# Kernel optimization log

Measured on AMD Instinct MI355X. Metric: run time of the kernel, lower is better.

The kernel has to match this reference:

```python
import jax, jax.numpy as jnp
import numpy as np

IN_CH = 4
HIDDEN = 32
NNODES = 4
N_NODES_TOTAL = 4_000_000
N_EDGES = 12_000_000


def setup_inputs() -> dict:
    key = jax.random.key(0)
    ks = jax.random.split(key, 8)
    state = jax.random.normal(ks[0], (N_NODES_TOTAL, IN_CH), dtype=jnp.float32)
    edge_index = jax.random.randint(ks[1], (2, N_EDGES), 0, N_NODES_TOTAL, dtype=jnp.int64)
    s = 1.0 / np.sqrt(IN_CH)
    W_gcn = jax.random.uniform(ks[2], (IN_CH, HIDDEN), jnp.float32, -s, s)
    b_gcn = jnp.zeros((HIDDEN,), jnp.float32)
    d_in1 = IN_CH + HIDDEN
    s1 = 1.0 / np.sqrt(d_in1)
    W1 = jax.random.uniform(ks[3], (d_in1, HIDDEN), jnp.float32, -s1, s1)
    b1 = jax.random.uniform(ks[4], (HIDDEN,), jnp.float32, -s1, s1)
    s2 = 1.0 / np.sqrt(HIDDEN)
    W2 = jax.random.uniform(ks[5], (HIDDEN, 1), jnp.float32, -s2, s2)
    b2 = jax.random.uniform(ks[6], (1,), jnp.float32, -s2, s2)
    return {"state": state, "edge_index": edge_index, "W_gcn": W_gcn,
            "b_gcn": b_gcn, "W1": W1, "b1": b1, "W2": W2, "b2": b2}


def gcn_conv(x, edge_index, W, b):
    # PyG GCNConv: linear transform, add self-loops, symmetric deg normalization,
    # scatter-add messages src -> dst, then bias.
    N = x.shape[0]
    loops = jnp.arange(N, dtype=edge_index.dtype)
    src = jnp.concatenate([edge_index[0], loops])
    dst = jnp.concatenate([edge_index[1], loops])
    xw = x @ W  # [N, HIDDEN]
    deg = jnp.zeros((N,), xw.dtype).at[dst].add(jnp.ones((), xw.dtype))
    dinv = jax.lax.rsqrt(deg)  # deg >= 1 thanks to self-loops
    norm = dinv[src] * dinv[dst]  # [E+N]
    out = jnp.zeros_like(xw).at[dst].add(norm[:, None] * xw[src])
    return out + b


def reference(state, edge_index, W_gcn, b_gcn, W1, b1, W2, b2):
    x_pp = gcn_conv(state, edge_index, W_gcn, b_gcn)          # [N, HIDDEN]
    x_pp = jnp.concatenate([state, x_pp], axis=1)              # [N, IN_CH+HIDDEN]
    x_pp = x_pp.reshape(-1, NNODES, IN_CH + HIDDEN)            # [B, nnodes, F]
    v = jnp.sum(x_pp, axis=1)                                  # [B, F] sum-pool over nodes
    v = jax.nn.relu(v @ W1 + b1)
    v = v @ W2 + b2
    return v.squeeze(-1)                                       # [B]
```

## Files before the change

kernel.cpp:

```cpp
#include <hip/hip_runtime.h>
#include <hip/hip_cooperative_groups.h>

namespace cg = cooperative_groups;

typedef unsigned long long u64;
typedef __attribute__((ext_vector_type(4))) int i32x4;
typedef __attribute__((ext_vector_type(2))) unsigned long long u64x2;

#define N_NODES   4000000
#define N_EDGES   12000000
#define N_GRAPHS  1000000

#define NBIN      977
#define GPBIN     1024
#define NPBIN     4096
#define BINCAP    14336
#define LCAP      16
#define SBLOCKS   256
#define SEPB      46880


__global__ __launch_bounds__(256) void fold_kernel(
    const float* __restrict__ Wgcn, const float* __restrict__ bgcn,
    const float* __restrict__ W1, const float* __restrict__ b1,
    float* __restrict__ fold) {
  int t = threadIdx.x;
  if (t < 128) {
    int j = t >> 2, c = t & 3;
    float s = 0.f;
    for (int k = 0; k < 32; ++k) s += Wgcn[c * 32 + k] * W1[(4 + k) * 32 + j];
    fold[j * 4 + c] = s;
  }
  if (t < 32) {
    float s = 0.f;
    for (int k = 0; k < 32; ++k) s += bgcn[k] * W1[(4 + k) * 32 + t];
    fold[128 + t] = b1[t] + 4.0f * s;
  }
}


__global__ __launch_bounds__(512) void binscatter_kernel(
    const int* __restrict__ src, const int* __restrict__ dst,
    unsigned* __restrict__ gcur, u64* __restrict__ recs) {
  extern __shared__ char smem[];
  u64* buf = (u64*)smem;
  unsigned* cnt = (unsigned*)(smem + NBIN * LCAP * 8);
  int t = threadIdx.x;
  for (int i = t; i < NBIN; i += 512) cnt[i] = 0;
  __syncthreads();
  const int base = blockIdx.x * SEPB;
  const int limit = min(SEPB, N_EDGES - base);
  const int V = limit >> 2;
  const i32x4* src4 = (const i32x4*)(src + base);
  const i32x4* dst4 = (const i32x4*)(dst + base);
  const int nrounds = (V + 1023) / 1024;

  i32x4 cs0 = {0,0,0,0}, cd0 = {0,0,0,0}, cs1 = {0,0,0,0}, cd1 = {0,0,0,0};
  {
    int i0 = t, i1 = t + 512;
    if (i0 < V) { cs0 = __builtin_nontemporal_load(src4 + i0);
                  cd0 = __builtin_nontemporal_load(dst4 + i0); }
    if (i1 < V) { cs1 = __builtin_nontemporal_load(src4 + i1);
                  cd1 = __builtin_nontemporal_load(dst4 + i1); }
  }
  for (int r = 0; r < nrounds; ++r) {
    i32x4 ns0 = {0,0,0,0}, nd0 = {0,0,0,0}, ns1 = {0,0,0,0}, nd1 = {0,0,0,0};
    if (r + 1 < nrounds) {
      int j0 = (r + 1) * 1024 + t, j1 = j0 + 512;
      if (j0 < V) { ns0 = __builtin_nontemporal_load(src4 + j0);
                    nd0 = __builtin_nontemporal_load(dst4 + j0); }
      if (j1 < V) { ns1 = __builtin_nontemporal_load(src4 + j1);
                    nd1 = __builtin_nontemporal_load(dst4 + j1); }
    }
    int idx0 = r * 1024 + t;
#pragma unroll
    for (int half = 0; half < 2; ++half) {
      int idx = idx0 + half * 512;
      if (idx < V) {
        i32x4 vs = half ? cs1 : cs0;
        i32x4 vd = half ? cd1 : cd0;
#pragma unroll
        for (int k = 0; k < 4; ++k) {
          int s = vs[k];
          int d = vd[k];
          unsigned graph = (unsigned)d >> 2;
          unsigned bin   = graph >> 10;
          unsigned glo   = graph & 1023u;
          u64 rec = ((u64)glo << 32) | ((u64)((unsigned)s << 2) | (unsigned)(d & 3));
          unsigned pos = atomicAdd(&cnt[bin], 1u);
          if (pos < LCAP) buf[bin * LCAP + pos] = rec;
          else {
            unsigned p = atomicAdd(&gcur[bin], 1u);
            if (p < BINCAP) recs[(size_t)bin * BINCAP + p] = rec;
          }
        }
      }
    }
    __syncthreads();
    bool fin = (r == nrounds - 1);
    for (int bin = t; bin < NBIN; bin += 512) {
      unsigned c = cnt[bin]; if (c > LCAP) c = LCAP;
      unsigned nn = fin ? c : (c & ~7u);
      if (nn) {
        unsigned pos = atomicAdd(&gcur[bin], nn);
        if (pos + nn <= BINCAP) {
          u64* dp = recs + (size_t)bin * BINCAP + pos;
          for (unsigned i2 = 0; i2 < nn; ++i2) dp[i2] = buf[bin * LCAP + i2];
        }
      }
      unsigned rem2 = c - nn;
      for (unsigned i2 = 0; i2 < rem2; ++i2)
        buf[bin * LCAP + i2] = buf[bin * LCAP + nn + i2];
      cnt[bin] = rem2;
    }
    __syncthreads();
    cs0 = ns0; cd0 = nd0; cs1 = ns1; cd1 = nd1;
  }
}


__global__ __launch_bounds__(512, 8) void fusedreduce_kernel(
    const u64* __restrict__ recs, const unsigned* __restrict__ gcur,
    float4* __restrict__ dsi4, const float4* __restrict__ state4,
    const float* __restrict__ W1, const float* __restrict__ fold,
    const float* __restrict__ W2, const float* __restrict__ b2,
    float* __restrict__ out) {
  extern __shared__ float dynsm[];
  unsigned* degL = (unsigned*)dynsm;
  float* dinvL = dynsm;
  float* accL  = dynsm + NPBIN;
  __shared__ float4 w1aT[32], wg1T[32];
  __shared__ float b1p[32], w2s[32];
  int t = threadIdx.x, bin = blockIdx.x;
  if (t < 32) {
    w1aT[t] = make_float4(W1[t], W1[32 + t], W1[64 + t], W1[96 + t]);
    wg1T[t] = ((const float4*)fold)[t];
    b1p[t]  = fold[128 + t];
    w2s[t]  = W2[t];
  }
  for (int i = t; i < NPBIN; i += 512) { degL[i] = 0u; accL[i] = 0.f; }
  __syncthreads();
  unsigned n = gcur[bin]; if (n > BINCAP) n = BINCAP;
  const u64* rp = recs + (size_t)bin * BINCAP;
  {
    const u64x2* rv = (const u64x2*)rp;
    unsigned nv = n >> 1;
    for (unsigned i = t; i < nv; i += 512) {
      u64x2 p = __builtin_nontemporal_load(rv + i);
      atomicAdd(&degL[((unsigned)(p.x >> 32)) * 4 + ((unsigned)p.x & 3u)], 1u);
      atomicAdd(&degL[((unsigned)(p.y >> 32)) * 4 + ((unsigned)p.y & 3u)], 1u);
    }
    if ((n & 1u) && t == 0) {
      u64 v = rp[n - 1];
      atomicAdd(&degL[((unsigned)(v >> 32)) * 4 + ((unsigned)v & 3u)], 1u);
    }
  }
  __syncthreads();
  int nb = bin * NPBIN;
  for (int i = t; i < NPBIN; i += 512) {
    int node = nb + i;
    float dv = rsqrtf((float)(degL[i] + 1u));
    dinvL[i] = dv;
    if (node < N_NODES) {
      float4 s = state4[node];
      dsi4[node] = make_float4(dv * s.x, dv * s.y, dv * s.z, dv * s.w);
    }
  }
  __threadfence();
  cg::this_grid().sync();
  unsigned q = n >> 2;
  for (unsigned i = t; i < q; i += 512) {
    u64 r0 = __builtin_nontemporal_load(rp + i);
    u64 r1 = __builtin_nontemporal_load(rp + i + q);
    u64 r2 = __builtin_nontemporal_load(rp + i + 2 * q);
    u64 r3 = __builtin_nontemporal_load(rp + i + 3 * q);
    unsigned lo0 = (unsigned)r0, g0 = (unsigned)(r0 >> 32), s0 = lo0 >> 2;
    unsigned lo1 = (unsigned)r1, g1 = (unsigned)(r1 >> 32), s1 = lo1 >> 2;
    unsigned lo2 = (unsigned)r2, g2 = (unsigned)(r2 >> 32), s2 = lo2 >> 2;
    unsigned lo3 = (unsigned)r3, g3 = (unsigned)(r3 >> 32), s3 = lo3 >> 2;
    float w0 = dinvL[g0 * 4 + (lo0 & 3u)];
    float w1 = dinvL[g1 * 4 + (lo1 & 3u)];
    float w2 = dinvL[g2 * 4 + (lo2 & 3u)];
    float w3 = dinvL[g3 * 4 + (lo3 & 3u)];
    float4 m0 = dsi4[s0], m1 = dsi4[s1], m2 = dsi4[s2], m3 = dsi4[s3];
    float* a;
    a = accL + g0 * 4;
    atomicAdd(a + 0, w0 * m0.x); atomicAdd(a + 1, w0 * m0.y);
    atomicAdd(a + 2, w0 * m0.z); atomicAdd(a + 3, w0 * m0.w);
    a = accL + g1 * 4;
    atomicAdd(a + 0, w1 * m1.x); atomicAdd(a + 1, w1 * m1.y);
    atomicAdd(a + 2, w1 * m1.z); atomicAdd(a + 3, w1 * m1.w);
    a = accL + g2 * 4;
    atomicAdd(a + 0, w2 * m2.x); atomicAdd(a + 1, w2 * m2.y);
    atomicAdd(a + 2, w2 * m2.z); atomicAdd(a + 3, w2 * m2.w);
    a = accL + g3 * 4;
    atomicAdd(a + 0, w3 * m3.x); atomicAdd(a + 1, w3 * m3.y);
    atomicAdd(a + 2, w3 * m3.z); atomicAdd(a + 3, w3 * m3.w);
  }
  {
    unsigned done = q << 2;
    unsigned rem = n - done;
    if ((unsigned)t < rem) {
      u64 v = rp[done + t];
      unsigned lo = (unsigned)v, g = (unsigned)(v >> 32), s = lo >> 2;
      float w = dinvL[g * 4 + (lo & 3u)];
      float4 mm = dsi4[s];
      float* a = accL + g * 4;
      atomicAdd(a + 0, w * mm.x); atomicAdd(a + 1, w * mm.y);
      atomicAdd(a + 2, w * mm.z); atomicAdd(a + 3, w * mm.w);
    }
  }
  __syncthreads();
  for (int gi = t; gi < GPBIN; gi += 512) {
    int g = bin * GPBIN + gi;
    if (g >= N_GRAPHS) break;
    float4 s0 = state4[4 * g + 0], s1 = state4[4 * g + 1];
    float4 s2 = state4[4 * g + 2], s3 = state4[4 * g + 3];
    float d0 = dinvL[gi * 4 + 0], d1 = dinvL[gi * 4 + 1];
    float d2 = dinvL[gi * 4 + 2], d3 = dinvL[gi * 4 + 3];
    float q0 = d0 * d0, q1 = d1 * d1, q2 = d2 * d2, q3 = d3 * d3;
    float ax = accL[gi * 4 + 0] + q0 * s0.x + q1 * s1.x + q2 * s2.x + q3 * s3.x;
    float ay = accL[gi * 4 + 1] + q0 * s0.y + q1 * s1.y + q2 * s2.y + q3 * s3.y;
    float az = accL[gi * 4 + 2] + q0 * s0.z + q1 * s1.z + q2 * s2.z + q3 * s3.z;
    float aw = accL[gi * 4 + 3] + q0 * s0.w + q1 * s1.w + q2 * s2.w + q3 * s3.w;
    float vx = s0.x + s1.x + s2.x + s3.x;
    float vy = s0.y + s1.y + s2.y + s3.y;
    float vz = s0.z + s1.z + s2.z + s3.z;
    float vw = s0.w + s1.w + s2.w + s3.w;
    float accum = b2[0];
#pragma unroll 4
    for (int j = 0; j < 32; ++j) {
      float4 wa = w1aT[j], wg = wg1T[j];
      float h = b1p[j]
              + vx * wa.x + vy * wa.y + vz * wa.z + vw * wa.w
              + ax * wg.x + ay * wg.y + az * wg.z + aw * wg.w;
      accum += fmaxf(h, 0.f) * w2s[j];
    }
    out[g] = accum;
  }
}


__global__ __launch_bounds__(512) void bindeg_kernel(
    const u64* __restrict__ recs, const unsigned* __restrict__ gcur,
    const float4* __restrict__ state4,
    float* __restrict__ dinv, float4* __restrict__ dsi4) {
  __shared__ unsigned degL[NPBIN];
  int t = threadIdx.x, bin = blockIdx.x;
  for (int i = t; i < NPBIN; i += 512) degL[i] = 0;
  __syncthreads();
  unsigned n = gcur[bin]; if (n > BINCAP) n = BINCAP;
  const u64* rp = recs + (size_t)bin * BINCAP;
  const u64x2* rv = (const u64x2*)rp;
  unsigned nv = n >> 1;
  for (unsigned i = t; i < nv; i += 512) {
    u64x2 p = __builtin_nontemporal_load(rv + i);
    atomicAdd(&degL[((unsigned)(p.x >> 32)) * 4 + ((unsigned)p.x & 3u)], 1u);
    atomicAdd(&degL[((unsigned)(p.y >> 32)) * 4 + ((unsigned)p.y & 3u)], 1u);
  }
  if ((n & 1u) && t == 0) {
    u64 v = rp[n - 1];
    atomicAdd(&degL[((unsigned)(v >> 32)) * 4 + ((unsigned)v & 3u)], 1u);
  }
  __syncthreads();
  int nb = bin * NPBIN;
  for (int i = t; i < NPBIN; i += 512) {
    int node = nb + i;
    if (node < N_NODES) {
      float dv = rsqrtf((float)(degL[i] + 1u));
      dinv[node] = dv;
      float4 s = state4[node];
      dsi4[node] = make_float4(dv * s.x, dv * s.y, dv * s.z, dv * s.w);
    }
  }
}

__global__ __launch_bounds__(512, 8) void binreduce_kernel(
    const u64* __restrict__ recs, const unsigned* __restrict__ gcur,
    const float* __restrict__ dinv, const float4* __restrict__ dsi4,
    const float4* __restrict__ state4,
    const float* __restrict__ W1, const float* __restrict__ fold,
    const float* __restrict__ W2, const float* __restrict__ b2,
    float* __restrict__ out) {
  extern __shared__ float dynsm[];
  float* dinvL = dynsm;
  float* accL  = dynsm + NPBIN;
  __shared__ float4 w1aT[32], wg1T[32];
  __shared__ float b1p[32], w2s[32];
  int t = threadIdx.x, bin = blockIdx.x;
  if (t < 32) {
    w1aT[t] = make_float4(W1[t], W1[32 + t], W1[64 + t], W1[96 + t]);
    wg1T[t] = ((const float4*)fold)[t];
    b1p[t]  = fold[128 + t];
    w2s[t]  = W2[t];
  }
  int nb = bin * NPBIN;
  for (int i = t; i < NPBIN; i += 512) {
    int node = nb + i;
    dinvL[i] = (node < N_NODES) ? dinv[node] : 0.f;
    accL[i]  = 0.f;
  }
  __syncthreads();
  unsigned n = gcur[bin]; if (n > BINCAP) n = BINCAP;
  const u64* rp = recs + (size_t)bin * BINCAP;
  unsigned q = n >> 2;
  for (unsigned i = t; i < q; i += 512) {
    u64 r0 = __builtin_nontemporal_load(rp + i);
    u64 r1 = __builtin_nontemporal_load(rp + i + q);
    u64 r2 = __builtin_nontemporal_load(rp + i + 2 * q);
    u64 r3 = __builtin_nontemporal_load(rp + i + 3 * q);
    unsigned lo0 = (unsigned)r0, g0 = (unsigned)(r0 >> 32), s0 = lo0 >> 2;
    unsigned lo1 = (unsigned)r1, g1 = (unsigned)(r1 >> 32), s1 = lo1 >> 2;
    unsigned lo2 = (unsigned)r2, g2 = (unsigned)(r2 >> 32), s2 = lo2 >> 2;
    unsigned lo3 = (unsigned)r3, g3 = (unsigned)(r3 >> 32), s3 = lo3 >> 2;
    float w0 = dinvL[g0 * 4 + (lo0 & 3u)];
    float w1 = dinvL[g1 * 4 + (lo1 & 3u)];
    float w2 = dinvL[g2 * 4 + (lo2 & 3u)];
    float w3 = dinvL[g3 * 4 + (lo3 & 3u)];
    float4 m0 = dsi4[s0], m1 = dsi4[s1], m2 = dsi4[s2], m3 = dsi4[s3];
    float* a;
    a = accL + g0 * 4;
    atomicAdd(a + 0, w0 * m0.x); atomicAdd(a + 1, w0 * m0.y);
    atomicAdd(a + 2, w0 * m0.z); atomicAdd(a + 3, w0 * m0.w);
    a = accL + g1 * 4;
    atomicAdd(a + 0, w1 * m1.x); atomicAdd(a + 1, w1 * m1.y);
    atomicAdd(a + 2, w1 * m1.z); atomicAdd(a + 3, w1 * m1.w);
    a = accL + g2 * 4;
    atomicAdd(a + 0, w2 * m2.x); atomicAdd(a + 1, w2 * m2.y);
    atomicAdd(a + 2, w2 * m2.z); atomicAdd(a + 3, w2 * m2.w);
    a = accL + g3 * 4;
    atomicAdd(a + 0, w3 * m3.x); atomicAdd(a + 1, w3 * m3.y);
    atomicAdd(a + 2, w3 * m3.z); atomicAdd(a + 3, w3 * m3.w);
  }
  unsigned done = q << 2;
  unsigned rem = n - done;
  if ((unsigned)t < rem) {
    u64 v = rp[done + t];
    unsigned lo = (unsigned)v, g = (unsigned)(v >> 32), s = lo >> 2;
    float w = dinvL[g * 4 + (lo & 3u)];
    float4 mm = dsi4[s];
    float* a = accL + g * 4;
    atomicAdd(a + 0, w * mm.x); atomicAdd(a + 1, w * mm.y);
    atomicAdd(a + 2, w * mm.z); atomicAdd(a + 3, w * mm.w);
  }
  __syncthreads();
  for (int gi = t; gi < GPBIN; gi += 512) {
    int g = bin * GPBIN + gi;
    if (g >= N_GRAPHS) break;
    float4 s0 = state4[4 * g + 0], s1 = state4[4 * g + 1];
    float4 s2 = state4[4 * g + 2], s3 = state4[4 * g + 3];
    float d0 = dinvL[gi * 4 + 0], d1 = dinvL[gi * 4 + 1];
    float d2 = dinvL[gi * 4 + 2], d3 = dinvL[gi * 4 + 3];
    float q0 = d0 * d0, q1 = d1 * d1, q2 = d2 * d2, q3 = d3 * d3;
    float ax = accL[gi * 4 + 0] + q0 * s0.x + q1 * s1.x + q2 * s2.x + q3 * s3.x;
    float ay = accL[gi * 4 + 1] + q0 * s0.y + q1 * s1.y + q2 * s2.y + q3 * s3.y;
    float az = accL[gi * 4 + 2] + q0 * s0.z + q1 * s1.z + q2 * s2.z + q3 * s3.z;
    float aw = accL[gi * 4 + 3] + q0 * s0.w + q1 * s1.w + q2 * s2.w + q3 * s3.w;
    float vx = s0.x + s1.x + s2.x + s3.x;
    float vy = s0.y + s1.y + s2.y + s3.y;
    float vz = s0.z + s1.z + s2.z + s3.z;
    float vw = s0.w + s1.w + s2.w + s3.w;
    float accum = b2[0];
#pragma unroll 4
    for (int j = 0; j < 32; ++j) {
      float4 wa = w1aT[j], wg = wg1T[j];
      float h = b1p[j]
              + vx * wa.x + vy * wa.y + vz * wa.z + vw * wa.w
              + ax * wg.x + ay * wg.y + az * wg.z + aw * wg.w;
      accum += fmaxf(h, 0.f) * w2s[j];
    }
    out[g] = accum;
  }
}


__global__ __launch_bounds__(256) void deg_kernel(
    const i32x4* __restrict__ dst4, unsigned* __restrict__ deg) {
  int stride = gridDim.x * blockDim.x;
  for (int e = blockIdx.x * blockDim.x + threadIdx.x; e < N_EDGES / 4; e += stride) {
    i32x4 d = __builtin_nontemporal_load(dst4 + e);
    atomicAdd(&deg[d.x], 1u); atomicAdd(&deg[d.y], 1u);
    atomicAdd(&deg[d.z], 1u); atomicAdd(&deg[d.w], 1u);
  }
}

__global__ __launch_bounds__(256) void dinv_kernel(unsigned* __restrict__ degdinv) {
  int i = blockIdx.x * blockDim.x + threadIdx.x;
  if (i < N_NODES) {
    float dv = rsqrtf((float)(degdinv[i] + 1u));
    reinterpret_cast<float*>(degdinv)[i] = dv;
  }
}

__global__ __launch_bounds__(256) void scatter_kernel(
    const i32x4* __restrict__ src4, const i32x4* __restrict__ dst4,
    const float* __restrict__ dinv, const float4* __restrict__ state4,
    float* __restrict__ acc) {
  int stride = gridDim.x * blockDim.x;
  for (int e = blockIdx.x * blockDim.x + threadIdx.x; e < N_EDGES / 4; e += stride) {
    i32x4 s4 = __builtin_nontemporal_load(src4 + e);
    i32x4 d4 = __builtin_nontemporal_load(dst4 + e);
#pragma unroll
    for (int u = 0; u < 4; ++u) {
      int s = (u == 0) ? s4.x : (u == 1) ? s4.y : (u == 2) ? s4.z : s4.w;
      int d = (u == 0) ? d4.x : (u == 1) ? d4.y : (u == 2) ? d4.z : d4.w;
      float w = dinv[s] * dinv[d];
      float4 st = state4[s];
      float* base = acc + (size_t)(d >> 2) * 4;
      atomicAdd(base + 0, w * st.x); atomicAdd(base + 1, w * st.y);
      atomicAdd(base + 2, w * st.z); atomicAdd(base + 3, w * st.w);
    }
  }
}

__global__ __launch_bounds__(256) void final_kernel(
    const float4* __restrict__ state4, const float4* __restrict__ dinv4,
    const float4* __restrict__ acc4, const float* __restrict__ W1,
    const float* __restrict__ fold, const float* __restrict__ W2,
    const float* __restrict__ b2, float* __restrict__ out) {
  __shared__ float4 w1aT[32], wg1T[32];
  __shared__ float b1p[32], w2s[32];
  int t = threadIdx.x;
  if (t < 32) {
    w1aT[t] = make_float4(W1[t], W1[32 + t], W1[64 + t], W1[96 + t]);
    wg1T[t] = ((const float4*)fold)[t];
    b1p[t]  = fold[128 + t];
    w2s[t]  = W2[t];
  }
  __syncthreads();
  int b = blockIdx.x * blockDim.x + t;
  if (b >= N_GRAPHS) return;
  float4 s0 = state4[4 * b + 0], s1 = state4[4 * b + 1];
  float4 s2 = state4[4 * b + 2], s3 = state4[4 * b + 3];
  float4 dv = dinv4[b];
  float4 a  = acc4[b];
  float q0 = dv.x * dv.x, q1 = dv.y * dv.y, q2 = dv.z * dv.z, q3 = dv.w * dv.w;
  a.x += q0 * s0.x + q1 * s1.x + q2 * s2.x + q3 * s3.x;
  a.y += q0 * s0.y + q1 * s1.y + q2 * s2.y + q3 * s3.y;
  a.z += q0 * s0.z + q1 * s1.z + q2 * s2.z + q3 * s3.z;
  a.w += q0 * s0.w + q1 * s1.w + q2 * s2.w + q3 * s3.w;
  float4 vs;
  vs.x = s0.x + s1.x + s2.x + s3.x;
  vs.y = s0.y + s1.y + s2.y + s3.y;
  vs.z = s0.z + s1.z + s2.z + s3.z;
  vs.w = s0.w + s1.w + s2.w + s3.w;
  float accum = b2[0];
#pragma unroll
  for (int j = 0; j < 32; ++j) {
    float4 wa = w1aT[j], wg = wg1T[j];
    float h = b1p[j]
            + vs.x * wa.x + vs.y * wa.y + vs.z * wa.z + vs.w * wa.w
            + a.x * wg.x + a.y * wg.y + a.z * wg.z + a.w * wg.w;
    accum += fmaxf(h, 0.f) * w2s[j];
  }
  out[b] = accum;
}


extern "C" void kernel_launch(void* const* d_in, const int* in_sizes, int n_in,
                              void* d_out, int out_size, void* d_ws, size_t ws_size,
                              hipStream_t stream) {
  const float* state = (const float*)d_in[0];
  const int*   ei    = (const int*)d_in[1];
  const float* Wgcn  = (const float*)d_in[2];
  const float* bgcn  = (const float*)d_in[3];
  const float* W1    = (const float*)d_in[4];
  const float* b1    = (const float*)d_in[5];
  const float* W2    = (const float*)d_in[6];
  const float* b2    = (const float*)d_in[7];
  float* out = (float*)d_out;

  char* ws = (char*)d_ws;
  const size_t MB = 1024u * 1024u;

  const size_t recs_bytes = (size_t)NBIN * BINCAP * 8;
  const size_t dinv_off   = recs_bytes;
  const size_t dsi_off    = dinv_off + (size_t)N_NODES * 4;
  const size_t gcur_off   = (dsi_off + (size_t)N_NODES * 16 + 255) & ~(size_t)255;
  const size_t need_bin   = gcur_off + 8192 + 1024;

  const size_t scat_smem = (size_t)NBIN * LCAP * 8 + NBIN * 4;
  const size_t red_smem  = 2 * NPBIN * 4;

  if (ws_size >= need_bin) {
    const u64*      recs = (const u64*)ws;
    u64*            recsw = (u64*)ws;
    float*          dinv = (float*)(ws + dinv_off);
    float4*         dsi4 = (float4*)(ws + dsi_off);
    unsigned*       gcur = (unsigned*)(ws + gcur_off);
    float*          fold = (float*)(ws + gcur_off + 8192);
    const float4*   state4 = (const float4*)state;

    (void)hipMemsetAsync(gcur, 0, 8192, stream);
    fold_kernel<<<1, 128, 0, stream>>>(Wgcn, bgcn, W1, b1, fold);
    binscatter_kernel<<<SBLOCKS, 512, scat_smem, stream>>>(
        ei, ei + N_EDGES, gcur, recsw);

    bool coop_ok = false;
    {
      int dev = 0;
      (void)hipGetDevice(&dev);
      int coop_attr = 0;
      (void)hipDeviceGetAttribute(&coop_attr, hipDeviceAttributeCooperativeLaunch, dev);
      int numCU = 0;
      (void)hipDeviceGetAttribute(&numCU, hipDeviceAttributeMultiprocessorCount, dev);
      int maxblk = 0;
      hipError_t oe = hipOccupancyMaxActiveBlocksPerMultiprocessor(
          &maxblk, fusedreduce_kernel, 512, red_smem);
      if (coop_attr && oe == hipSuccess && (long)maxblk * numCU >= NBIN) {
        const float* W1p = W1; const float* foldp = fold;
        const float* W2p = W2; const float* b2p = b2;
        void* args[] = {(void*)&recs, (void*)&gcur, (void*)&dsi4, (void*)&state4,
                        (void*)&W1p, (void*)&foldp, (void*)&W2p, (void*)&b2p,
                        (void*)&out};
        hipError_t le = hipLaunchCooperativeKernel(
            fusedreduce_kernel, dim3(NBIN), dim3(512), args,
            (unsigned)red_smem, stream);
        coop_ok = (le == hipSuccess);
      }
    }
    if (!coop_ok) {
      bindeg_kernel<<<NBIN, 512, 0, stream>>>(recs, gcur, state4, dinv, dsi4);
      binreduce_kernel<<<NBIN, 512, red_smem, stream>>>(
          recs, gcur, dinv, dsi4, state4, W1, fold, W2, b2, out);
    }
    return;
  }

  {
    unsigned* deg  = (unsigned*)ws;
    float*    acc  = (float*)(ws + 16 * MB);
    float*    fold = (float*)(ws + 32 * MB);
    (void)hipMemsetAsync(d_ws, 0, 32 * MB + 1024, stream);
    fold_kernel<<<1, 128, 0, stream>>>(Wgcn, bgcn, W1, b1, fold);
    deg_kernel<<<4096, 256, 0, stream>>>((const i32x4*)(ei + N_EDGES), deg);
    dinv_kernel<<<(N_NODES + 255) / 256, 256, 0, stream>>>(deg);
    scatter_kernel<<<8192, 256, 0, stream>>>(
        (const i32x4*)ei, (const i32x4*)(ei + N_EDGES),
        (const float*)deg, (const float4*)state, acc);
    final_kernel<<<(N_GRAPHS + 255) / 256, 256, 0, stream>>>(
        (const float4*)state, (const float4*)deg, (const float4*)acc,
        W1, fold, W2, b2, out);
  }
}
```

Before: 429.7 us.

## Pack edge records into 32-bit words with finer 256-graph sub-bins

Edge records shrink from 64-bit to 32-bit words by packing the local graph id (8 bits), source node and slot into one word. Bins are subdivided into 3907 sub-bins of 256 graphs each, which the reduce kernels read four at a time as quads. This halves the record traffic written by the scatter and read twice by the reduce. The cost is many more shared-memory staging bins with a smaller per-bin buffer (LCAP 9) and a larger shared allocation, which may mean more small global flushes and lower scatter occupancy.

```diff
diff --git a/kernel.cpp b/kernel.cpp
--- a/kernel.cpp
+++ b/kernel.cpp
@@ -3,21 +3,19 @@
 
 namespace cg = cooperative_groups;
 
-typedef unsigned long long u64;
 typedef __attribute__((ext_vector_type(4))) int i32x4;
-typedef __attribute__((ext_vector_type(2))) unsigned long long u64x2;
 
 #define N_NODES   4000000
 #define N_EDGES   12000000
 #define N_GRAPHS  1000000
 
-#define NBIN      977
-#define GPBIN     1024
-#define NPBIN     4096
-#define BINCAP    14336
-#define LCAP      16
+#define NMB       3907
+#define MBCAP     4096
+#define LCAP      9
 #define SBLOCKS   256
 #define SEPB      46880
+#define NQUAD     977
+
 
 
 __global__ __launch_bounds__(256) void fold_kernel(
@@ -41,12 +39,12 @@
 
 __global__ __launch_bounds__(512) void binscatter_kernel(
     const int* __restrict__ src, const int* __restrict__ dst,
-    unsigned* __restrict__ gcur, u64* __restrict__ recs) {
+    unsigned* __restrict__ gcur, unsigned* __restrict__ recs) {
   extern __shared__ char smem[];
-  u64* buf = (u64*)smem;
-  unsigned* cnt = (unsigned*)(smem + NBIN * LCAP * 8);
+  unsigned* buf = (unsigned*)smem;
+  unsigned* cnt = (unsigned*)(smem + NMB * LCAP * 4);
   int t = threadIdx.x;
-  for (int i = t; i < NBIN; i += 512) cnt[i] = 0;
+  for (int i = t; i < NMB; i += 512) cnt[i] = 0;
   __syncthreads();
   const int base = blockIdx.x * SEPB;
   const int limit = min(SEPB, N_EDGES - base);
@@ -81,30 +79,29 @@
         i32x4 vd = half ? cd1 : cd0;
 #pragma unroll
         for (int k = 0; k < 4; ++k) {
-          int s = vs[k];
-          int d = vd[k];
-          unsigned graph = (unsigned)d >> 2;
-          unsigned bin   = graph >> 10;
-          unsigned glo   = graph & 1023u;
-          u64 rec = ((u64)glo << 32) | ((u64)((unsigned)s << 2) | (unsigned)(d & 3));
+          unsigned s = (unsigned)vs[k];
+          unsigned d = (unsigned)vd[k];
+          unsigned graph = d >> 2;
+          unsigned bin   = graph >> 8;
+          unsigned rec = ((graph & 255u) << 24) | (s << 2) | (d & 3u);
           unsigned pos = atomicAdd(&cnt[bin], 1u);
           if (pos < LCAP) buf[bin * LCAP + pos] = rec;
           else {
             unsigned p = atomicAdd(&gcur[bin], 1u);
-            if (p < BINCAP) recs[(size_t)bin * BINCAP + p] = rec;
+            if (p < MBCAP) recs[(size_t)bin * MBCAP + p] = rec;
           }
         }
       }
     }
     __syncthreads();
     bool fin = (r == nrounds - 1);
-    for (int bin = t; bin < NBIN; bin += 512) {
+    for (int bin = t; bin < NMB; bin += 512) {
       unsigned c = cnt[bin]; if (c > LCAP) c = LCAP;
       unsigned nn = fin ? c : (c & ~7u);
       if (nn) {
         unsigned pos = atomicAdd(&gcur[bin], nn);
-        if (pos + nn <= BINCAP) {
-          u64* dp = recs + (size_t)bin * BINCAP + pos;
+        if (pos + nn <= MBCAP) {
+          unsigned* dp = recs + (size_t)bin * MBCAP + pos;
           for (unsigned i2 = 0; i2 < nn; ++i2) dp[i2] = buf[bin * LCAP + i2];
         }
       }
@@ -120,7 +117,7 @@
 
 
 __global__ __launch_bounds__(512, 8) void fusedreduce_kernel(
-    const u64* __restrict__ recs, const unsigned* __restrict__ gcur,
+    const unsigned* __restrict__ recs, const unsigned* __restrict__ gcur,
     float4* __restrict__ dsi4, const float4* __restrict__ state4,
     const float* __restrict__ W1, const float* __restrict__ fold,
     const float* __restrict__ W2, const float* __restrict__ b2,
@@ -128,36 +125,41 @@
   extern __shared__ float dynsm[];
   unsigned* degL = (unsigned*)dynsm;
   float* dinvL = dynsm;
-  float* accL  = dynsm + NPBIN;
+  float* accL  = dynsm + 4096;
   __shared__ float4 w1aT[32], wg1T[32];
   __shared__ float b1p[32], w2s[32];
-  int t = threadIdx.x, bin = blockIdx.x;
+  int t = threadIdx.x, qb = blockIdx.x;
   if (t < 32) {
     w1aT[t] = make_float4(W1[t], W1[32 + t], W1[64 + t], W1[96 + t]);
     wg1T[t] = ((const float4*)fold)[t];
     b1p[t]  = fold[128 + t];
     w2s[t]  = W2[t];
   }
-  for (int i = t; i < NPBIN; i += 512) { degL[i] = 0u; accL[i] = 0.f; }
-  __syncthreads();
-  unsigned n = gcur[bin]; if (n > BINCAP) n = BINCAP;
-  const u64* rp = recs + (size_t)bin * BINCAP;
-  {
-    const u64x2* rv = (const u64x2*)rp;
-    unsigned nv = n >> 1;
-    for (unsigned i = t; i < nv; i += 512) {
-      u64x2 p = __builtin_nontemporal_load(rv + i);
-      atomicAdd(&degL[((unsigned)(p.x >> 32)) * 4 + ((unsigned)p.x & 3u)], 1u);
-      atomicAdd(&degL[((unsigned)(p.y >> 32)) * 4 + ((unsigned)p.y & 3u)], 1u);
-    }
-    if ((n & 1u) && t == 0) {
-      u64 v = rp[n - 1];
-      atomicAdd(&degL[((unsigned)(v >> 32)) * 4 + ((unsigned)v & 3u)], 1u);
-    }
-  }
-  __syncthreads();
-  int nb = bin * NPBIN;
-  for (int i = t; i < NPBIN; i += 512) {
+  for (int i = t; i < 4096; i += 512) { degL[i] = 0u; accL[i] = 0.f; }
+  __syncthreads();
+  unsigned n[4];
+  const unsigned* rp[4];
+#pragma unroll
+  for (int s = 0; s < 4; ++s) {
+    int mb = qb * 4 + s;
+    unsigned c = (mb < NMB) ? gcur[mb] : 0u;
+    n[s] = (c > MBCAP) ? (unsigned)MBCAP : c;
+    rp[s] = recs + (size_t)mb * MBCAP;
+  }
+  unsigned mx = max(max(n[0], n[1]), max(n[2], n[3]));
+  for (unsigned i = t; i < mx; i += 512) {
+#pragma unroll
+    for (int s = 0; s < 4; ++s) {
+      if (i < n[s]) {
+        unsigned r = __builtin_nontemporal_load(rp[s] + i);
+        unsigned lg = (unsigned)(s * 256) + (r >> 24);
+        atomicAdd(&degL[lg * 4 + (r & 3u)], 1u);
+      }
+    }
+  }
+  __syncthreads();
+  int nb = qb * 4096;
+  for (int i = t; i < 4096; i += 512) {
     int node = nb + i;
     float dv = rsqrtf((float)(degL[i] + 1u));
     dinvL[i] = dv;
@@ -168,51 +170,49 @@
   }
   __threadfence();
   cg::this_grid().sync();
-  unsigned q = n >> 2;
-  for (unsigned i = t; i < q; i += 512) {
-    u64 r0 = __builtin_nontemporal_load(rp + i);
-    u64 r1 = __builtin_nontemporal_load(rp + i + q);
-    u64 r2 = __builtin_nontemporal_load(rp + i + 2 * q);
-    u64 r3 = __builtin_nontemporal_load(rp + i + 3 * q);
-    unsigned lo0 = (unsigned)r0, g0 = (unsigned)(r0 >> 32), s0 = lo0 >> 2;
-    unsigned lo1 = (unsigned)r1, g1 = (unsigned)(r1 >> 32), s1 = lo1 >> 2;
-    unsigned lo2 = (unsigned)r2, g2 = (unsigned)(r2 >> 32), s2 = lo2 >> 2;
-    unsigned lo3 = (unsigned)r3, g3 = (unsigned)(r3 >> 32), s3 = lo3 >> 2;
-    float w0 = dinvL[g0 * 4 + (lo0 & 3u)];
-    float w1 = dinvL[g1 * 4 + (lo1 & 3u)];
-    float w2 = dinvL[g2 * 4 + (lo2 & 3u)];
-    float w3 = dinvL[g3 * 4 + (lo3 & 3u)];
-    float4 m0 = dsi4[s0], m1 = dsi4[s1], m2 = dsi4[s2], m3 = dsi4[s3];
-    float* a;
-    a = accL + g0 * 4;
-    atomicAdd(a + 0, w0 * m0.x); atomicAdd(a + 1, w0 * m0.y);
-    atomicAdd(a + 2, w0 * m0.z); atomicAdd(a + 3, w0 * m0.w);
-    a = accL + g1 * 4;
-    atomicAdd(a + 0, w1 * m1.x); atomicAdd(a + 1, w1 * m1.y);
-    atomicAdd(a + 2, w1 * m1.z); atomicAdd(a + 3, w1 * m1.w);
-    a = accL + g2 * 4;
-    atomicAdd(a + 0, w2 * m2.x); atomicAdd(a + 1, w2 * m2.y);
-    atomicAdd(a + 2, w2 * m2.z); atomicAdd(a + 3, w2 * m2.w);
-    a = accL + g3 * 4;
-    atomicAdd(a + 0, w3 * m3.x); atomicAdd(a + 1, w3 * m3.y);
-    atomicAdd(a + 2, w3 * m3.z); atomicAdd(a + 3, w3 * m3.w);
-  }
-  {
-    unsigned done = q << 2;
-    unsigned rem = n - done;
-    if ((unsigned)t < rem) {
-      u64 v = rp[done + t];
-      unsigned lo = (unsigned)v, g = (unsigned)(v >> 32), s = lo >> 2;
-      float w = dinvL[g * 4 + (lo & 3u)];
-      float4 mm = dsi4[s];
-      float* a = accL + g * 4;
-      atomicAdd(a + 0, w * mm.x); atomicAdd(a + 1, w * mm.y);
-      atomicAdd(a + 2, w * mm.z); atomicAdd(a + 3, w * mm.w);
-    }
-  }
-  __syncthreads();
-  for (int gi = t; gi < GPBIN; gi += 512) {
-    int g = bin * GPBIN + gi;
+  for (unsigned i = t; i < mx; i += 512) {
+    unsigned r0 = 0, r1 = 0, r2 = 0, r3 = 0;
+    bool v0 = i < n[0], v1 = i < n[1], v2 = i < n[2], v3 = i < n[3];
+    if (v0) r0 = __builtin_nontemporal_load(rp[0] + i);
+    if (v1) r1 = __builtin_nontemporal_load(rp[1] + i);
+    if (v2) r2 = __builtin_nontemporal_load(rp[2] + i);
+    if (v3) r3 = __builtin_nontemporal_load(rp[3] + i);
+    if (v0) {
+      unsigned lg = (r0 >> 24), src = (r0 >> 2) & 0x3FFFFFu;
+      float w = dinvL[lg * 4 + (r0 & 3u)];
+      float4 m = dsi4[src];
+      float* a = accL + lg * 4;
+      atomicAdd(a + 0, w * m.x); atomicAdd(a + 1, w * m.y);
+      atomicAdd(a + 2, w * m.z); atomicAdd(a + 3, w * m.w);
+    }
+    if (v1) {
+      unsigned lg = 256u + (r1 >> 24), src = (r1 >> 2) & 0x3FFFFFu;
+      float w = dinvL[lg * 4 + (r1 & 3u)];
+      float4 m = dsi4[src];
+      float* a = accL + lg * 4;
+      atomicAdd(a + 0, w * m.x); atomicAdd(a + 1, w * m.y);
+      atomicAdd(a + 2, w * m.z); atomicAdd(a + 3, w * m.w);
+    }
+    if (v2) {
+      unsigned lg = 512u + (r2 >> 24), src = (r2 >> 2) & 0x3FFFFFu;
+      float w = dinvL[lg * 4 + (r2 & 3u)];
+      float4 m = dsi4[src];
+      float* a = accL + lg * 4;
+      atomicAdd(a + 0, w * m.x); atomicAdd(a + 1, w * m.y);
+      atomicAdd(a + 2, w * m.z); atomicAdd(a + 3, w * m.w);
+    }
+    if (v3) {
+      unsigned lg = 768u + (r3 >> 24), src = (r3 >> 2) & 0x3FFFFFu;
+      float w = dinvL[lg * 4 + (r3 & 3u)];
+      float4 m = dsi4[src];
+      float* a = accL + lg * 4;
+      atomicAdd(a + 0, w * m.x); atomicAdd(a + 1, w * m.y);
+      atomicAdd(a + 2, w * m.z); atomicAdd(a + 3, w * m.w);
+    }
+  }
+  __syncthreads();
+  for (int gi = t; gi < 1024; gi += 512) {
+    int g = qb * 1024 + gi;
     if (g >= N_GRAPHS) break;
     float4 s0 = state4[4 * g + 0], s1 = state4[4 * g + 1];
     float4 s2 = state4[4 * g + 2], s3 = state4[4 * g + 3];
@@ -242,29 +242,27 @@
 
 
 __global__ __launch_bounds__(512) void bindeg_kernel(
-    const u64* __restrict__ recs, const unsigned* __restrict__ gcur,
+    const unsigned* __restrict__ recs, const unsigned* __restrict__ gcur,
     const float4* __restrict__ state4,
     float* __restrict__ dinv, float4* __restrict__ dsi4) {
-  __shared__ unsigned degL[NPBIN];
-  int t = threadIdx.x, bin = blockIdx.x;
-  for (int i = t; i < NPBIN; i += 512) degL[i] = 0;
-  __syncthreads();
-  unsigned n = gcur[bin]; if (n > BINCAP) n = BINCAP;
-  const u64* rp = recs + (size_t)bin * BINCAP;
-  const u64x2* rv = (const u64x2*)rp;
-  unsigned nv = n >> 1;
-  for (unsigned i = t; i < nv; i += 512) {
-    u64x2 p = __builtin_nontemporal_load(rv + i);
-    atomicAdd(&degL[((unsigned)(p.x >> 32)) * 4 + ((unsigned)p.x & 3u)], 1u);
-    atomicAdd(&degL[((unsigned)(p.y >> 32)) * 4 + ((unsigned)p.y & 3u)], 1u);
-  }
-  if ((n & 1u) && t == 0) {
-    u64 v = rp[n - 1];
-    atomicAdd(&degL[((unsigned)(v >> 32)) * 4 + ((unsigned)v & 3u)], 1u);
-  }
-  __syncthreads();
-  int nb = bin * NPBIN;
-  for (int i = t; i < NPBIN; i += 512) {
+  __shared__ unsigned degL[4096];
+  int t = threadIdx.x, qb = blockIdx.x;
+  for (int i = t; i < 4096; i += 512) degL[i] = 0;
+  __syncthreads();
+  for (int s = 0; s < 4; ++s) {
+    int mb = qb * 4 + s;
+    unsigned c = (mb < NMB) ? gcur[mb] : 0u;
+    unsigned nn = (c > MBCAP) ? (unsigned)MBCAP : c;
+    const unsigned* rp = recs + (size_t)mb * MBCAP;
+    for (unsigned i = t; i < nn; i += 512) {
+      unsigned r = __builtin_nontemporal_load(rp + i);
+      unsigned lg = (unsigned)(s * 256) + (r >> 24);
+      atomicAdd(&degL[lg * 4 + (r & 3u)], 1u);
+    }
+  }
+  __syncthreads();
+  int nb = qb * 4096;
+  for (int i = t; i < 4096; i += 512) {
     int node = nb + i;
     if (node < N_NODES) {
       float dv = rsqrtf((float)(degL[i] + 1u));
@@ -276,7 +274,7 @@
 }
 
 __global__ __launch_bounds__(512, 8) void binreduce_kernel(
-    const u64* __restrict__ recs, const unsigned* __restrict__ gcur,
+    const unsigned* __restrict__ recs, const unsigned* __restrict__ gcur,
     const float* __restrict__ dinv, const float4* __restrict__ dsi4,
     const float4* __restrict__ state4,
     const float* __restrict__ W1, const float* __restrict__ fold,
@@ -284,68 +282,76 @@
     float* __restrict__ out) {
   extern __shared__ float dynsm[];
   float* dinvL = dynsm;
-  float* accL  = dynsm + NPBIN;
+  float* accL  = dynsm + 4096;
   __shared__ float4 w1aT[32], wg1T[32];
   __shared__ float b1p[32], w2s[32];
-  int t = threadIdx.x, bin = blockIdx.x;
+  int t = threadIdx.x, qb = blockIdx.x;
   if (t < 32) {
     w1aT[t] = make_float4(W1[t], W1[32 + t], W1[64 + t], W1[96 + t]);
     wg1T[t] = ((const float4*)fold)[t];
     b1p[t]  = fold[128 + t];
     w2s[t]  = W2[t];
   }
-  int nb = bin * NPBIN;
-  for (int i = t; i < NPBIN; i += 512) {
+  int nb = qb * 4096;
+  for (int i = t; i < 4096; i += 512) {
     int node = nb + i;
     dinvL[i] = (node < N_NODES) ? dinv[node] : 0.f;
     accL[i]  = 0.f;
   }
   __syncthreads();
-  unsigned n = gcur[bin]; if (n > BINCAP) n = BINCAP;
-  const u64* rp = recs + (size_t)bin * BINCAP;
-  unsigned q = n >> 2;
-  for (unsigned i = t; i < q; i += 512) {
-    u64 r0 = __builtin_nontemporal_load(rp + i);
-    u64 r1 = __builtin_nontemporal_load(rp + i + q);
-    u64 r2 = __builtin_nontemporal_load(rp + i + 2 * q);
-    u64 r3 = __builtin_nontemporal_load(rp + i + 3 * q);
-    unsigned lo0 = (unsigned)r0, g0 = (unsigned)(r0 >> 32), s0 = lo0 >> 2;
-    unsigned lo1 = (unsigned)r1, g1 = (unsigned)(r1 >> 32), s1 = lo1 >> 2;
-    unsigned lo2 = (unsigned)r2, g2 = (unsigned)(r2 >> 32), s2 = lo2 >> 2;
-    unsigned lo3 = (unsigned)r3, g3 = (unsigned)(r3 >> 32), s3 = lo3 >> 2;
-    float w0 = dinvL[g0 * 4 + (lo0 & 3u)];
-    float w1 = dinvL[g1 * 4 + (lo1 & 3u)];
-    float w2 = dinvL[g2 * 4 + (lo2 & 3u)];
-    float w3 = dinvL[g3 * 4 + (lo3 & 3u)];
-    float4 m0 = dsi4[s0], m1 = dsi4[s1], m2 = dsi4[s2], m3 = dsi4[s3];
-    float* a;
-    a = accL + g0 * 4;
-    atomicAdd(a + 0, w0 * m0.x); atomicAdd(a + 1, w0 * m0.y);
-    atomicAdd(a + 2, w0 * m0.z); atomicAdd(a + 3, w0 * m0.w);
-    a = accL + g1 * 4;
-    atomicAdd(a + 0, w1 * m1.x); atomicAdd(a + 1, w1 * m1.y);
-    atomicAdd(a + 2, w1 * m1.z); atomicAdd(a + 3, w1 * m1.w);
-    a = accL + g2 * 4;
-    atomicAdd(a + 0, w2 * m2.x); atomicAdd(a + 1, w2 * m2.y);
-    atomicAdd(a + 2, w2 * m2.z); atomicAdd(a + 3, w2 * m2.w);
-    a = accL + g3 * 4;
-    atomicAdd(a + 0, w3 * m3.x); atomicAdd(a + 1, w3 * m3.y);
-    atomicAdd(a + 2, w3 * m3.z); atomicAdd(a + 3, w3 * m3.w);
-  }
-  unsigned done = q << 2;
-  unsigned rem = n - done;
-  if ((unsigned)t < rem) {
-    u64 v = rp[done + t];
-    unsigned lo = (unsigned)v, g = (unsigned)(v >> 32), s = lo >> 2;
-    float w = dinvL[g * 4 + (lo & 3u)];
-    float4 mm = dsi4[s];
-    float* a = accL + g * 4;
-    atomicAdd(a + 0, w * mm.x); atomicAdd(a + 1, w * mm.y);
-    atomicAdd(a + 2, w * mm.z); atomicAdd(a + 3, w * mm.w);
-  }
-  __syncthreads();
-  for (int gi = t; gi < GPBIN; gi += 512) {
-    int g = bin * GPBIN + gi;
+  unsigned n[4];
+  const unsigned* rp[4];
+#pragma unroll
+  for (int s = 0; s < 4; ++s) {
+    int mb = qb * 4 + s;
+    unsigned c = (mb < NMB) ? gcur[mb] : 0u;
+    n[s] = (c > MBCAP) ? (unsigned)MBCAP : c;
+    rp[s] = recs + (size_t)mb * MBCAP;
+  }
+  unsigned mx = max(max(n[0], n[1]), max(n[2], n[3]));
+  for (unsigned i = t; i < mx; i += 512) {
+    unsigned r0 = 0, r1 = 0, r2 = 0, r3 = 0;
+    bool v0 = i < n[0], v1 = i < n[1], v2 = i < n[2], v3 = i < n[3];
+    if (v0) r0 = __builtin_nontemporal_load(rp[0] + i);
+    if (v1) r1 = __builtin_nontemporal_load(rp[1] + i);
+    if (v2) r2 = __builtin_nontemporal_load(rp[2] + i);
+    if (v3) r3 = __builtin_nontemporal_load(rp[3] + i);
+    if (v0) {
+      unsigned lg = (r0 >> 24), src = (r0 >> 2) & 0x3FFFFFu;
+      float w = dinvL[lg * 4 + (r0 & 3u)];
+      float4 m = dsi4[src];
+      float* a = accL + lg * 4;
+      atomicAdd(a + 0, w * m.x); atomicAdd(a + 1, w * m.y);
+      atomicAdd(a + 2, w * m.z); atomicAdd(a + 3, w * m.w);
+    }
+    if (v1) {
+      unsigned lg = 256u + (r1 >> 24), src = (r1 >> 2) & 0x3FFFFFu;
+      float w = dinvL[lg * 4 + (r1 & 3u)];
+      float4 m = dsi4[src];
+      float* a = accL + lg * 4;
+      atomicAdd(a + 0, w * m.x); atomicAdd(a + 1, w * m.y);
+      atomicAdd(a + 2, w * m.z); atomicAdd(a + 3, w * m.w);
+    }
+    if (v2) {
+      unsigned lg = 512u + (r2 >> 24), src = (r2 >> 2) & 0x3FFFFFu;
+      float w = dinvL[lg * 4 + (r2 & 3u)];
+      float4 m = dsi4[src];
+      float* a = accL + lg * 4;
+      atomicAdd(a + 0, w * m.x); atomicAdd(a + 1, w * m.y);
+      atomicAdd(a + 2, w * m.z); atomicAdd(a + 3, w * m.w);
+    }
+    if (v3) {
+      unsigned lg = 768u + (r3 >> 24), src = (r3 >> 2) & 0x3FFFFFu;
+      float w = dinvL[lg * 4 + (r3 & 3u)];
+      float4 m = dsi4[src];
+      float* a = accL + lg * 4;
+      atomicAdd(a + 0, w * m.x); atomicAdd(a + 1, w * m.y);
+      atomicAdd(a + 2, w * m.z); atomicAdd(a + 3, w * m.w);
+    }
+  }
+  __syncthreads();
+  for (int gi = t; gi < 1024; gi += 512) {
+    int g = qb * 1024 + gi;
     if (g >= N_GRAPHS) break;
     float4 s0 = state4[4 * g + 0], s1 = state4[4 * g + 1];
     float4 s2 = state4[4 * g + 2], s3 = state4[4 * g + 3];
@@ -473,28 +479,30 @@
   char* ws = (char*)d_ws;
   const size_t MB = 1024u * 1024u;
 
-  const size_t recs_bytes = (size_t)NBIN * BINCAP * 8;
+  const size_t recs_bytes = (size_t)NMB * MBCAP * 4;
   const size_t dinv_off   = recs_bytes;
   const size_t dsi_off    = dinv_off + (size_t)N_NODES * 4;
   const size_t gcur_off   = (dsi_off + (size_t)N_NODES * 16 + 255) & ~(size_t)255;
-  const size_t need_bin   = gcur_off + 8192 + 1024;
-
-  const size_t scat_smem = (size_t)NBIN * LCAP * 8 + NBIN * 4;
-  const size_t red_smem  = 2 * NPBIN * 4;
+  const size_t need_bin   = gcur_off + 16384 + 1024;
+
+  const size_t scat_smem = (size_t)NMB * LCAP * 4 + NMB * 4;
+  const size_t red_smem  = 2 * 4096 * 4;
 
   if (ws_size >= need_bin) {
-    const u64*      recs = (const u64*)ws;
-    u64*            recsw = (u64*)ws;
+    unsigned*       recs = (unsigned*)ws;
     float*          dinv = (float*)(ws + dinv_off);
     float4*         dsi4 = (float4*)(ws + dsi_off);
     unsigned*       gcur = (unsigned*)(ws + gcur_off);
-    float*          fold = (float*)(ws + gcur_off + 8192);
+    float*          fold = (float*)(ws + gcur_off + 16384);
     const float4*   state4 = (const float4*)state;
 
-    (void)hipMemsetAsync(gcur, 0, 8192, stream);
+    (void)hipFuncSetAttribute((const void*)binscatter_kernel,
+        hipFuncAttributeMaxDynamicSharedMemorySize, 160 * 1024);
+
+    (void)hipMemsetAsync(gcur, 0, 16384, stream);
     fold_kernel<<<1, 128, 0, stream>>>(Wgcn, bgcn, W1, b1, fold);
     binscatter_kernel<<<SBLOCKS, 512, scat_smem, stream>>>(
-        ei, ei + N_EDGES, gcur, recsw);
+        ei, ei + N_EDGES, gcur, recs);
 
     bool coop_ok = false;
     {
@@ -507,21 +515,23 @@
       int maxblk = 0;
       hipError_t oe = hipOccupancyMaxActiveBlocksPerMultiprocessor(
           &maxblk, fusedreduce_kernel, 512, red_smem);
-      if (coop_attr && oe == hipSuccess && (long)maxblk * numCU >= NBIN) {
+      if (coop_attr && oe == hipSuccess && (long)maxblk * numCU >= NQUAD) {
+        const unsigned* recsc = recs;
+        const unsigned* gcurc = gcur;
         const float* W1p = W1; const float* foldp = fold;
         const float* W2p = W2; const float* b2p = b2;
-        void* args[] = {(void*)&recs, (void*)&gcur, (void*)&dsi4, (void*)&state4,
+        void* args[] = {(void*)&recsc, (void*)&gcurc, (void*)&dsi4, (void*)&state4,
                         (void*)&W1p, (void*)&foldp, (void*)&W2p, (void*)&b2p,
                         (void*)&out};
         hipError_t le = hipLaunchCooperativeKernel(
-            fusedreduce_kernel, dim3(NBIN), dim3(512), args,
+            fusedreduce_kernel, dim3(NQUAD), dim3(512), args,
             (unsigned)red_smem, stream);
         coop_ok = (le == hipSuccess);
       }
     }
     if (!coop_ok) {
-      bindeg_kernel<<<NBIN, 512, 0, stream>>>(recs, gcur, state4, dinv, dsi4);
-      binreduce_kernel<<<NBIN, 512, red_smem, stream>>>(
+      bindeg_kernel<<<NQUAD, 512, 0, stream>>>(recs, gcur, state4, dinv, dsi4);
+      binreduce_kernel<<<NQUAD, 512, red_smem, stream>>>(
           recs, gcur, dinv, dsi4, state4, W1, fold, W2, b2, out);
     }
     return;
```

New measurement: 474.4 us. +10.4%, slower.
